# Kernel optimization log

Measured on AMD Instinct MI355X. Metric: run time of the kernel, lower is better.

Reference implementation:

```python
import jax, jax.numpy as jnp
import numpy as np

B, S, D, H, V = 4, 2048, 128, 4, 64
HD = D // H
ITERS = 3
SCALE = 1.0 / float(np.sqrt(HD))
APO = 0.2
TRP = 0.15
FC = 1.61803
EPS = 1e-5


def ln(x, g, b):
    m = x.mean(-1, keepdims=True)
    v = ((x - m) ** 2).mean(-1, keepdims=True)
    return (x - m) / jnp.sqrt(v + EPS) * g + b


def setup_inputs() -> dict:
    key = jax.random.key(0)
    ks = iter(jax.random.split(key, 64))

    def w(shape, s=0.02):
        return jax.random.normal(next(ks), shape, jnp.float32) * s

    return {
        "x": jax.random.normal(next(ks), (B, S, D), jnp.float32),
        "space": jax.random.normal(next(ks), (B, S, D), jnp.float32),
        # attn_norm
        "g_attn": jnp.ones(D), "b_attn": jnp.zeros(D),
        # RecursiveScaledDotProductAttention
        "Wq": w((D, D)), "Wk": w((D, D)), "Wv": w((D, D)),
        "Wo": w((D, D)), "bo": jnp.zeros(D),
        "Wg": w((D, 2 * D)), "bg": jnp.zeros(D),
        "Wobs": w((H, D)), "bobs": jnp.zeros(H),
        # trp_norm + TraumaResolutionPathLayer
        "g_trp": jnp.ones(D), "b_trp": jnp.zeros(D),
        "Wt": w((V, D)), "bt": jnp.zeros(V),
        "Wc": w((V, D)), "bc": jnp.zeros(V),
        "Ws": w((V, D)), "bs": jnp.zeros(V),
        "Wr": w((V, 3 * V)), "br": jnp.zeros(V),
        "fv": jnp.ones(V) * FC,
        "Wop": w((D, V)), "bop": jnp.zeros(D),
        # MorphogenesisFFN
        "g_ffn": jnp.ones(D), "b_ffn": jnp.zeros(D),
        "W1": w((4 * D, D)), "b1": jnp.zeros(4 * D),
        "W2": w((D, 4 * D)), "b2": jnp.zeros(D),
        "Wsg": w((D, D)), "bsg": jnp.zeros(D),
        # ApophasisLayer
        "g_apo": jnp.ones(D), "b_apo": jnp.zeros(D),
        "Wn": w((D, D)), "bn": jnp.zeros(D),
    }


def reference(x, space, g_attn, b_attn, Wq, Wk, Wv, Wo, bo, Wg, bg, Wobs, bobs,
              g_trp, b_trp, Wt, bt, Wc, bc, Ws, bs, Wr, br, fv, Wop, bop,
              g_ffn, b_ffn, W1, b1, W2, b2, Wsg, bsg, g_apo, b_apo, Wn, bn):
    # --- recursive attention (autopoiesis loop, eval mode: dropout = identity) ---
    xn = ln(x, g_attn, b_attn)
    obs = xn.mean(1, keepdims=True)                      # [B,1,D] observer_state default
    infl = (obs @ Wobs.T + bobs).transpose(0, 2, 1)[..., None]  # [B,H,1,1] per-head bias
    cur = xn
    for _ in range(ITERS):
        q = (cur @ Wq.T).reshape(B, S, H, HD).transpose(0, 2, 1, 3)
        k = (cur @ Wk.T).reshape(B, S, H, HD).transpose(0, 2, 1, 3)
        v = (cur @ Wv.T).reshape(B, S, H, HD).transpose(0, 2, 1, 3)
        scores = jnp.einsum('bhqd,bhkd->bhqk', q, k) * SCALE + infl
        aw = jax.nn.softmax(scores, axis=-1)             # [B,H,S,S]
        ao = jnp.einsum('bhqk,bhkd->bhqd', aw, v).transpose(0, 2, 1, 3).reshape(B, S, D)
        out = ao @ Wo.T + bo
        gate = jax.nn.sigmoid(jnp.concatenate([cur, out], -1) @ Wg.T + bg)
        cur = cur * (1 - gate) + out * gate
    x = x + cur
    # --- Trauma Resolution Path ---
    xn2 = ln(x, g_trp, b_trp)
    tv = xn2 @ Wt.T + bt                                 # [B,S,V]
    cv = jnp.broadcast_to(xn2.mean(1, keepdims=True) @ Wc.T + bc, tv.shape)
    sv = space @ Ws.T + bs
    rgate = jax.nn.sigmoid(jnp.concatenate([tv, cv, sv], -1) @ Wr.T + br)
    cn = jnp.maximum(jnp.linalg.norm(cv, axis=-1, keepdims=True), 1e-8)
    sn = jnp.maximum(jnp.linalg.norm(sv, axis=-1, keepdims=True), 1e-8)
    align = (cv * sv).sum(-1, keepdims=True) / (cn * sn)
    resolved = tv + TRP * (-align * (fv - tv) * rgate)
    x = x + resolved @ Wop.T + bop
    # --- Morphogenesis FFN ---
    xn3 = ln(x, g_ffn, b_ffn)
    ff = jax.nn.gelu(xn3 @ W1.T + b1, approximate=False) @ W2.T + b2
    x = x + jax.nn.sigmoid(xn3 @ Wsg.T + bsg) * ff
    # --- Apophasis ---
    x = x - APO * jnp.tanh(ln(x, g_apo, b_apo) @ Wn.T + bn)
    return x, aw
```

## Files before the change

kernel.cpp:

```cpp
#include <hip/hip_runtime.h>
#include <cstdint>
#include <cstddef>


typedef unsigned short u16;
typedef __attribute__((ext_vector_type(8))) short short8;
typedef __attribute__((ext_vector_type(4))) float f32x4;
typedef __attribute__((ext_vector_type(2))) unsigned uint32x2;

#define B_ 4
#define S_ 2048
#define D_ 128
#define H_ 4
#define M_ 8192
#define SCALE2_ 0.25503472510324417f
#define APO_ 0.2f
#define TRP_ 0.15f
#define EPS_ 1e-5f

__device__ __forceinline__ float fexp2(float x){ return __builtin_amdgcn_exp2f(x); }

__device__ __forceinline__ u16 f2bf(float f){
  unsigned u = __float_as_uint(f);
  unsigned r = ((u >> 16) & 1u) + 0x7fffu;
  return (u16)((u + r) >> 16);
}
__device__ __forceinline__ float bf2f(u16 u){ return __uint_as_float(((unsigned)u) << 16); }
__device__ __forceinline__ float sigm(float x){ return 1.0f/(1.0f + __expf(-x)); }

__device__ __forceinline__ unsigned cvtpk_bf16(float lo, float hi){
  unsigned r;
  asm("v_cvt_pk_bf16_f32 %0, %1, %2" : "=v"(r) : "v"(lo), "v"(hi));
  return r;
}

#define LDS_BARRIER() __asm__ volatile("s_waitcnt lgkmcnt(0)\n\ts_barrier" ::: "memory")

struct WSrc { const float* s[13]; };
__global__ __launch_bounds__(256) void prep_k(WSrc w, u16* __restrict__ dst,
    const float* __restrict__ x_in, const float* __restrict__ g,
    const float* __restrict__ b, u16* __restrict__ cg0){
  if (blockIdx.x < 1168){
    int idx = blockIdx.x*256 + threadIdx.x;
    if (idx >= 299008) return;
    const int sz[13] = {16384,16384,16384,16384,32768,8192,8192,12288,8192,65536,65536,16384,16384};
    int off = idx;
    #pragma unroll
    for (int seg = 0; seg < 13; ++seg){
      if (off < sz[seg]) { dst[idx] = f2bf(w.s[seg][off]); return; }
      off -= sz[seg];
    }
  } else {
    int wv = threadIdx.x >> 6, lane = threadIdx.x & 63;
    int row = (blockIdx.x - 1168)*4 + wv;
    size_t rb = (size_t)row * D_;
    float v0 = x_in[rb + lane], v1 = x_in[rb + lane + 64];
    float s = v0 + v1;
    #pragma unroll
    for (int m = 1; m < 64; m <<= 1) s += __shfl_xor(s, m, 64);
    float mean = s * (1.0f/128.0f);
    float d0 = v0 - mean, d1 = v1 - mean;
    float vv = d0*d0 + d1*d1;
    #pragma unroll
    for (int m = 1; m < 64; m <<= 1) vv += __shfl_xor(vv, m, 64);
    float rstd = rsqrtf(vv * (1.0f/128.0f) + EPS_);
    cg0[rb + lane]      = f2bf(d0*rstd*g[lane]    + b[lane]);
    cg0[rb + lane + 64] = f2bf(d1*rstd*g[lane+64] + b[lane+64]);
  }
}

__global__ __launch_bounds__(256) void ln_kernel(const float* __restrict__ in0,
    const u16* __restrict__ in1bf, const float* __restrict__ g, const float* __restrict__ b,
    float* __restrict__ sumout, u16* __restrict__ ybf){
  int wv = threadIdx.x >> 6, lane = threadIdx.x & 63;
  int row = blockIdx.x*4 + wv;
  size_t rb = (size_t)row * D_;
  float v0 = in0[rb + lane], v1 = in0[rb + lane + 64];
  if (in1bf){ v0 += bf2f(in1bf[rb + lane]); v1 += bf2f(in1bf[rb + lane + 64]); }
  if (sumout){ sumout[rb + lane] = v0; sumout[rb + lane + 64] = v1; }
  float s = v0 + v1;
  #pragma unroll
  for (int m = 1; m < 64; m <<= 1) s += __shfl_xor(s, m, 64);
  float mean = s * (1.0f/128.0f);
  float d0 = v0 - mean, d1 = v1 - mean;
  float vv = d0*d0 + d1*d1;
  #pragma unroll
  for (int m = 1; m < 64; m <<= 1) vv += __shfl_xor(vv, m, 64);
  float rstd = rsqrtf(vv * (1.0f/128.0f) + EPS_);
  ybf[rb + lane]      = f2bf(d0*rstd*g[lane]    + b[lane]);
  ybf[rb + lane + 64] = f2bf(d1*rstd*g[lane+64] + b[lane+64]);
}

__global__ __launch_bounds__(256) void colmean_k(const u16* __restrict__ lnb,
    const float* __restrict__ Wc, const float* __restrict__ bc,
    float* __restrict__ cv, float* __restrict__ cn){
  __shared__ float red[2][128];
  __shared__ float cmS[128];
  int b = blockIdx.x;
  int d = threadIdx.x & 127, sc = threadIdx.x >> 7;
  const u16* pp = lnb + (size_t)b*S_*D_ + (size_t)sc*1024*D_ + d;
  float s = 0.f;
  #pragma unroll 8
  for (int i = 0; i < 1024; ++i) s += bf2f(pp[(size_t)i*D_]);
  red[sc][d] = s;
  __syncthreads();
  if (sc == 0) cmS[d] = (red[0][d] + red[1][d]) * (1.0f/2048.0f);
  __syncthreads();
  int tid = threadIdx.x;
  if (tid < 64){
    int n = tid;
    const float* wrow = Wc + n*D_;
    float sacc = bc[n];
    #pragma unroll 4
    for (int dd = 0; dd < D_; ++dd) sacc += cmS[dd]*wrow[dd];
    cv[b*64 + n] = sacc;
    float sq = sacc*sacc;
    #pragma unroll
    for (int m = 1; m < 64; m <<= 1) sq += __shfl_xor(sq, m, 64);
    if (n == 0) cn[b] = fmaxf(sqrtf(sq), 1e-8f);
  }
}

__global__ __launch_bounds__(256) void gemm_qkv(const u16* __restrict__ A,
    const u16* __restrict__ W, u16* __restrict__ qh, u16* __restrict__ kh, u16* __restrict__ vt){
  __shared__ u16 Asm[64*136];
  __shared__ u16 Bsm[64*136];
  const int m0 = blockIdx.x*64, n0 = blockIdx.y*64;
  int tid = threadIdx.x;
  int wv = tid >> 6, lane = tid & 63, quad = lane >> 4, l15 = lane & 15;
  int wm = wv >> 1, wn = wv & 1;
  {
    int sr = tid >> 2, cb = (tid & 3)*32;
    const u16* ag = A + (size_t)(m0 + sr)*128 + cb;
    const u16* bg = W + (size_t)(n0 + sr)*128 + cb;
    short8 a0 = *(const short8*)(ag + 0);
    short8 a1 = *(const short8*)(ag + 8);
    short8 a2 = *(const short8*)(ag + 16);
    short8 a3 = *(const short8*)(ag + 24);
    short8 b0 = *(const short8*)(bg + 0);
    short8 b1 = *(const short8*)(bg + 8);
    short8 b2 = *(const short8*)(bg + 16);
    short8 b3 = *(const short8*)(bg + 24);
    *(short8*)(Asm + sr*136 + cb + 0)  = a0;
    *(short8*)(Asm + sr*136 + cb + 8)  = a1;
    *(short8*)(Asm + sr*136 + cb + 16) = a2;
    *(short8*)(Asm + sr*136 + cb + 24) = a3;
    *(short8*)(Bsm + sr*136 + cb + 0)  = b0;
    *(short8*)(Bsm + sr*136 + cb + 8)  = b1;
    *(short8*)(Bsm + sr*136 + cb + 16) = b2;
    *(short8*)(Bsm + sr*136 + cb + 24) = b3;
  }
  LDS_BARRIER();
  f32x4 acc[2][2];
  #pragma unroll
  for (int i = 0; i < 2; ++i)
    #pragma unroll
    for (int j = 0; j < 2; ++j) acc[i][j] = (f32x4){0.f,0.f,0.f,0.f};
  #pragma unroll
  for (int k0 = 0; k0 < 128; k0 += 32){
    short8 af0 = *(const short8*)(Asm + (wm*32      + l15)*136 + k0 + quad*8);
    short8 af1 = *(const short8*)(Asm + (wm*32 + 16 + l15)*136 + k0 + quad*8);
    short8 bf0 = *(const short8*)(Bsm + (wn*32      + l15)*136 + k0 + quad*8);
    short8 bf1 = *(const short8*)(Bsm + (wn*32 + 16 + l15)*136 + k0 + quad*8);
    acc[0][0] = __builtin_amdgcn_mfma_f32_16x16x32_bf16(af0, bf0, acc[0][0], 0,0,0);
    acc[0][1] = __builtin_amdgcn_mfma_f32_16x16x32_bf16(af0, bf1, acc[0][1], 0,0,0);
    acc[1][0] = __builtin_amdgcn_mfma_f32_16x16x32_bf16(af1, bf0, acc[1][0], 0,0,0);
    acc[1][1] = __builtin_amdgcn_mfma_f32_16x16x32_bf16(af1, bf1, acc[1][1], 0,0,0);
  }
  #pragma unroll
  for (int ms = 0; ms < 2; ++ms)
    #pragma unroll
    for (int ns = 0; ns < 2; ++ns){
      int mb = m0 + wm*32 + ms*16 + quad*4;
      int nn = n0 + wn*32 + ns*16 + l15;
      int which = nn >> 7, col = nn & 127, h = col >> 5, hd = col & 31;
      f32x4 c = acc[ms][ns];
      #pragma unroll
      for (int r = 0; r < 4; ++r){
        int m = mb + r, b = m >> 11, s = m & 2047;
        if (which == 0)      qh[((size_t)(b*H_+h)*S_ + s)*32 + hd] = f2bf(c[r]);
        else if (which == 1) kh[((size_t)(b*H_+h)*S_ + s)*32 + hd] = f2bf(c[r]);
        else                 vt[((size_t)(b*H_+h)*32 + hd)*S_ + s] = f2bf(c[r]);
      }
    }
}

template<bool WRITE_AW>
__global__ __launch_bounds__(256) void attn_k(const u16* __restrict__ qh, const u16* __restrict__ kh,
    const u16* __restrict__ vT, u16* __restrict__ ao_bf, float* __restrict__ aw){
  __shared__ u16 Ks[2][128*40];
  __shared__ u16 Vs[2][32*136];
  __shared__ u16 Ps[4*16*136];
  int L = blockIdx.y*32 + blockIdx.x;
  int xcd = L & 7, j = L >> 3;
  int bh = 2*xcd + (j >> 5);
  int q0 = (j & 31)*64;
  int b = bh >> 2, h = bh & 3;
  int tid = threadIdx.x, wv = tid >> 6, lane = tid & 63, quad = lane >> 4, l15 = lane & 15;
  int qrow = q0 + wv*16 + l15;
  const size_t bhS = (size_t)bh * S_;
  short8 qf = *(const short8*)(qh + (bhS + qrow)*32 + quad*8);
  int krow = tid >> 1, kseg = (tid & 1)*16;
  const u16* kg = kh + (bhS + krow)*32 + kseg;
  int vrow = tid >> 3, vseg = (tid & 7)*16;
  const u16* vg = vT + ((size_t)bh*32 + vrow)*S_ + vseg;
  f32x4 zero = {0.f,0.f,0.f,0.f};
  f32x4 ao0 = zero, ao1 = zero;
  float lsum = 0.f, rinv = 1.0f;
  u16* PsW = Ps + wv*16*136;

  if constexpr (WRITE_AW){
    {
      short8 a0 = *(const short8*)(kg + 0);
      short8 a1 = *(const short8*)(kg + 8);
      *(short8*)(Ks[0] + krow*40 + kseg    ) = a0;
      *(short8*)(Ks[0] + krow*40 + kseg + 8) = a1;
    }
    #pragma unroll 2
    for (int t = 0; t < 16; ++t){
      LDS_BARRIER();
      short8 n0, n1;
      if (t < 15){
        n0 = *(const short8*)(kg + (size_t)(t+1)*4096 + 0);
        n1 = *(const short8*)(kg + (size_t)(t+1)*4096 + 8);
      }
      const u16* Kb = Ks[t & 1];
      #pragma unroll
      for (int jt = 0; jt < 8; ++jt){
        short8 kf = *(const short8*)(Kb + (jt*16 + l15)*40 + quad*8);
        f32x4 s = __builtin_amdgcn_mfma_f32_16x16x32_bf16(kf, qf, zero, 0,0,0);
        #pragma unroll
        for (int r = 0; r < 4; ++r) lsum += fexp2(s[r]*SCALE2_);
      }
      if (t < 15){
        u16* Kn = Ks[(t+1) & 1];
        *(short8*)(Kn + krow*40 + kseg    ) = n0;
        *(short8*)(Kn + krow*40 + kseg + 8) = n1;
      }
    }
    lsum += __shfl_xor(lsum, 16, 64);
    lsum += __shfl_xor(lsum, 32, 64);
    rinv = 1.0f / lsum;
  }

  {
    short8 a0 = *(const short8*)(kg + 0);
    short8 a1 = *(const short8*)(kg + 8);
    short8 b0 = *(const short8*)(vg + 0);
    short8 b1 = *(const short8*)(vg + 8);
    *(short8*)(Ks[0] + krow*40 + kseg    ) = a0;
    *(short8*)(Ks[0] + krow*40 + kseg + 8) = a1;
    *(short8*)(Vs[0] + vrow*136 + vseg    ) = b0;
    *(short8*)(Vs[0] + vrow*136 + vseg + 8) = b1;
  }
  #pragma unroll 2
  for (int t = 0; t < 16; ++t){
    LDS_BARRIER();
    short8 kn0, kn1, vn0, vn1;
    if (t < 15){
      kn0 = *(const short8*)(kg + (size_t)(t+1)*4096 + 0);
      kn1 = *(const short8*)(kg + (size_t)(t+1)*4096 + 8);
      vn0 = *(const short8*)(vg + (size_t)(t+1)*128 + 0);
      vn1 = *(const short8*)(vg + (size_t)(t+1)*128 + 8);
    }
    const u16* Kb = Ks[t & 1];
    const u16* Vb = Vs[t & 1];
    int k0 = t*128;
    #pragma unroll
    for (int jt = 0; jt < 8; ++jt){
      short8 kf = *(const short8*)(Kb + (jt*16 + l15)*40 + quad*8);
      f32x4 s = __builtin_amdgcn_mfma_f32_16x16x32_bf16(kf, qf, zero, 0,0,0);
      float pv[4];
      #pragma unroll
      for (int r = 0; r < 4; ++r){
        float e = fexp2(s[r]*SCALE2_);
        if constexpr (WRITE_AW) e *= rinv; else lsum += e;
        pv[r] = e;
      }
      if constexpr (WRITE_AW){
        f32x4 st = {pv[0], pv[1], pv[2], pv[3]};
        *(f32x4*)(aw + (bhS + qrow)*S_ + k0 + jt*16 + quad*4) = st;
      }
      uint32x2 pk;
      pk[0] = cvtpk_bf16(pv[0], pv[1]);
      pk[1] = cvtpk_bf16(pv[2], pv[3]);
      *(uint32x2*)(PsW + l15*136 + jt*16 + quad*4) = pk;
    }
    __asm__ volatile("s_waitcnt lgkmcnt(0)" ::: "memory");
    #pragma unroll
    for (int jg = 0; jg < 4; ++jg){
      short8 pf  = *(const short8*)(PsW + l15*136 + jg*32 + quad*8);
      short8 vf0 = *(const short8*)(Vb + (l15     )*136 + jg*32 + quad*8);
      short8 vf1 = *(const short8*)(Vb + (16 + l15)*136 + jg*32 + quad*8);
      ao0 = __builtin_amdgcn_mfma_f32_16x16x32_bf16(vf0, pf, ao0, 0,0,0);
      ao1 = __builtin_amdgcn_mfma_f32_16x16x32_bf16(vf1, pf, ao1, 0,0,0);
    }
    if (t < 15){
      u16* Kn = Ks[(t+1) & 1];
      u16* Vn = Vs[(t+1) & 1];
      *(short8*)(Kn + krow*40 + kseg    ) = kn0;
      *(short8*)(Kn + krow*40 + kseg + 8) = kn1;
      *(short8*)(Vn + vrow*136 + vseg    ) = vn0;
      *(short8*)(Vn + vrow*136 + vseg + 8) = vn1;
    }
  }

  if constexpr (!WRITE_AW){
    lsum += __shfl_xor(lsum, 16, 64);
    lsum += __shfl_xor(lsum, 32, 64);
    rinv = 1.0f / lsum;
  } else rinv = 1.0f;

  size_t rowbase = ((size_t)(b*S_ + qrow))*D_ + h*32;
  #pragma unroll
  for (int dt = 0; dt < 2; ++dt){
    f32x4 a = dt ? ao1 : ao0;
    uint32x2 pk;
    pk[0] = cvtpk_bf16(a[0]*rinv, a[1]*rinv);
    pk[1] = cvtpk_bf16(a[2]*rinv, a[3]*rinv);
    *(uint32x2*)(ao_bf + rowbase + dt*16 + quad*4) = pk;
  }
}

template<bool DO_QKV>
__global__ __launch_bounds__(256) void wqkv_k(const u16* __restrict__ cin,
    const u16* __restrict__ ao_bf, const u16* __restrict__ wo, const u16* __restrict__ wg,
    const u16* __restrict__ w3, const float* __restrict__ bo, const float* __restrict__ bg,
    u16* __restrict__ cout, u16* __restrict__ qh, u16* __restrict__ kh, u16* __restrict__ vt){
  __shared__ u16 aoS[16*136];
  __shared__ u16 cuS[16*136];
  __shared__ u16 outS[16*136];
  __shared__ u16 coS[16*136];
  const int m0 = blockIdx.x*16;
  int tid = threadIdx.x, wv = tid >> 6, lane = tid & 63, quad = lane >> 4, l15 = lane & 15;
  {
    int row = tid >> 4, seg = (tid & 15)*8;
    *(short8*)(aoS + row*136 + seg) = *(const short8*)(ao_bf + (size_t)(m0+row)*128 + seg);
    *(short8*)(cuS + row*136 + seg) = *(const short8*)(cin   + (size_t)(m0+row)*128 + seg);
  }
  __syncthreads();
  f32x4 oacc[2] = {(f32x4){0,0,0,0},(f32x4){0,0,0,0}};
  #pragma unroll
  for (int kc = 0; kc < 4; ++kc){
    short8 af = *(const short8*)(aoS + l15*136 + kc*32 + quad*8);
    #pragma unroll
    for (int nt = 0; nt < 2; ++nt){
      int n = wv*32 + nt*16 + l15;
      short8 bfv = *(const short8*)(wo + (size_t)n*128 + kc*32 + quad*8);
      oacc[nt] = __builtin_amdgcn_mfma_f32_16x16x32_bf16(af, bfv, oacc[nt], 0,0,0);
    }
  }
  #pragma unroll
  for (int nt = 0; nt < 2; ++nt){
    int n = wv*32 + nt*16 + l15;
    float bias = bo[n];
    #pragma unroll
    for (int r = 0; r < 4; ++r){
      int m = quad*4 + r;
      outS[m*136 + n] = f2bf(oacc[nt][r] + bias);
    }
  }
  __syncthreads();
  f32x4 gacc[2] = {(f32x4){0,0,0,0},(f32x4){0,0,0,0}};
  #pragma unroll
  for (int kc = 0; kc < 8; ++kc){
    short8 af = (kc < 4) ? *(const short8*)(cuS  + l15*136 + kc*32 + quad*8)
                         : *(const short8*)(outS + l15*136 + (kc-4)*32 + quad*8);
    #pragma unroll
    for (int nt = 0; nt < 2; ++nt){
      int n = wv*32 + nt*16 + l15;
      short8 bfv = *(const short8*)(wg + (size_t)n*256 + kc*32 + quad*8);
      gacc[nt] = __builtin_amdgcn_mfma_f32_16x16x32_bf16(af, bfv, gacc[nt], 0,0,0);
    }
  }
  #pragma unroll
  for (int nt = 0; nt < 2; ++nt){
    int n = wv*32 + nt*16 + l15;
    float biasg = bg[n], biaso = bo[n];
    #pragma unroll
    for (int r = 0; r < 4; ++r){
      int m = quad*4 + r;
      float g = sigm(gacc[nt][r] + biasg);
      float c = bf2f(cuS[m*136 + n]);
      float o = oacc[nt][r] + biaso;
      u16 val = f2bf(c + g*(o - c));
      cout[(size_t)(m0+m)*128 + n] = val;
      if constexpr (DO_QKV) coS[m*136 + n] = val;
    }
  }
  if constexpr (DO_QKV){
    __syncthreads();
    f32x4 qacc[6];
    #pragma unroll
    for (int i = 0; i < 6; ++i) qacc[i] = (f32x4){0,0,0,0};
    #pragma unroll
    for (int kc = 0; kc < 4; ++kc){
      short8 af = *(const short8*)(coS + l15*136 + kc*32 + quad*8);
      #pragma unroll
      for (int nt = 0; nt < 6; ++nt){
        int n = wv*96 + nt*16 + l15;
        short8 bfv = *(const short8*)(w3 + (size_t)n*128 + kc*32 + quad*8);
        qacc[nt] = __builtin_amdgcn_mfma_f32_16x16x32_bf16(af, bfv, qacc[nt], 0,0,0);
      }
    }
    #pragma unroll
    for (int nt = 0; nt < 6; ++nt){
      int nn = wv*96 + nt*16 + l15;
      int which = nn >> 7, col = nn & 127, h = col >> 5, hd = col & 31;
      #pragma unroll
      for (int r = 0; r < 4; ++r){
        int m = m0 + quad*4 + r, b = m >> 11, s = m & 2047;
        if (which == 0)      qh[((size_t)(b*H_+h)*S_ + s)*32 + hd] = f2bf(qacc[nt][r]);
        else if (which == 1) kh[((size_t)(b*H_+h)*S_ + s)*32 + hd] = f2bf(qacc[nt][r]);
        else                 vt[((size_t)(b*H_+h)*32 + hd)*S_ + s] = f2bf(qacc[nt][r]);
      }
    }
  }
}

__global__ __launch_bounds__(256) void uber_k(const u16* __restrict__ lnb,
    const float* __restrict__ space, const float* __restrict__ xbuf,
    const float* __restrict__ cv, const float* __restrict__ cn,
    const u16* __restrict__ wt, const float* __restrict__ bt,
    const u16* __restrict__ wsx, const float* __restrict__ bs,
    const u16* __restrict__ wr, const float* __restrict__ br, const float* __restrict__ fv,
    const u16* __restrict__ wop, const float* __restrict__ bop,
    const float* __restrict__ g_ffn, const float* __restrict__ b_ffn,
    const u16* __restrict__ w1, const float* __restrict__ b1,
    const u16* __restrict__ w2, const float* __restrict__ b2,
    const u16* __restrict__ wsg, const float* __restrict__ bsg,
    const float* __restrict__ g_apo, const float* __restrict__ b_apo,
    const u16* __restrict__ wn, const float* __restrict__ bn,
    float* __restrict__ out_x){
  __shared__ u16 xnS[16*136];
  __shared__ u16 spS[16*136];
  __shared__ u16 CcS[16*200];
  __shared__ float svF[16*64];
  __shared__ u16 RsS[16*72];
  __shared__ float xrF[16*128];
  __shared__ u16 midS[16*536];
  __shared__ float alignS[16];
  const int m0 = blockIdx.x*16;
  const int bidx = m0 >> 11;
  int tid = threadIdx.x, wv = tid >> 6, lane = tid & 63, quad = lane >> 4, l15 = lane & 15;

  {
    int row = tid >> 4, seg = (tid & 15)*8;
    *(short8*)(xnS + row*136 + seg) = *(const short8*)(lnb + (size_t)(m0+row)*128 + seg);
    const float* sp = space + (size_t)(m0+row)*128 + seg;
    short8 pk;
    #pragma unroll
    for (int i = 0; i < 8; ++i) pk[i] = (short)f2bf(sp[i]);
    *(short8*)(spS + row*136 + seg) = pk;
    f32x4 xa = *(const f32x4*)(xbuf + (size_t)(m0+row)*128 + seg);
    f32x4 xb = *(const f32x4*)(xbuf + (size_t)(m0+row)*128 + seg + 4);
    *(f32x4*)(xrF + row*128 + seg) = xa;
    *(f32x4*)(xrF + row*128 + seg + 4) = xb;
  }
  __syncthreads();

  f32x4 tvacc = {0,0,0,0};
  {
    int n = wv*16 + l15;
    #pragma unroll
    for (int kc = 0; kc < 4; ++kc){
      short8 af  = *(const short8*)(xnS + l15*136 + kc*32 + quad*8);
      short8 bfv = *(const short8*)(wt + (size_t)n*128 + kc*32 + quad*8);
      tvacc = __builtin_amdgcn_mfma_f32_16x16x32_bf16(af, bfv, tvacc, 0,0,0);
    }
    float bias = bt[n];
    #pragma unroll
    for (int r = 0; r < 4; ++r){
      tvacc[r] += bias;
      CcS[(quad*4 + r)*200 + n] = f2bf(tvacc[r]);
    }
  }
  {
    int n = wv*16 + l15;
    f32x4 sva = {0,0,0,0};
    #pragma unroll
    for (int kc = 0; kc < 4; ++kc){
      short8 af  = *(const short8*)(spS + l15*136 + kc*32 + quad*8);
      short8 bfv = *(const short8*)(wsx + (size_t)n*128 + kc*32 + quad*8);
      sva = __builtin_amdgcn_mfma_f32_16x16x32_bf16(af, bfv, sva, 0,0,0);
    }
    float bias = bs[n];
    #pragma unroll
    for (int r = 0; r < 4; ++r){
      float v = sva[r] + bias;
      int m = quad*4 + r;
      CcS[m*200 + 128 + n] = f2bf(v);
      svF[m*64 + n] = v;
    }
    int row = tid >> 4, c4 = (tid & 15)*4;
    #pragma unroll
    for (int i = 0; i < 4; ++i)
      CcS[row*200 + 64 + c4 + i] = f2bf(cv[bidx*64 + c4 + i]);
  }
  __syncthreads();

  {
    float cnb = cn[bidx];
    for (int rr = wv*4; rr < wv*4 + 4; ++rr){
      float s = svF[rr*64 + lane];
      float c = cv[bidx*64 + lane];
      float dot = c*s, ss = s*s;
      #pragma unroll
      for (int m = 1; m < 64; m <<= 1){ dot += __shfl_xor(dot, m, 64); ss += __shfl_xor(ss, m, 64); }
      if (lane == 0){
        float sn = fmaxf(sqrtf(ss), 1e-8f);
        alignS[rr] = dot / (cnb * sn);
      }
    }
  }
  __syncthreads();

  {
    int n = wv*16 + l15;
    f32x4 ra = {0,0,0,0};
    #pragma unroll
    for (int kc = 0; kc < 6; ++kc){
      short8 af  = *(const short8*)(CcS + l15*200 + kc*32 + quad*8);
      short8 bfv = *(const short8*)(wr + (size_t)n*192 + kc*32 + quad*8);
      ra = __builtin_amdgcn_mfma_f32_16x16x32_bf16(af, bfv, ra, 0,0,0);
    }
    float bias = br[n], fvn = fv[n];
    #pragma unroll
    for (int r = 0; r < 4; ++r){
      int m = quad*4 + r;
      float rg = sigm(ra[r] + bias);
      float t = tvacc[r];
      float res = t + TRP_*(-alignS[m]*(fvn - t)*rg);
      RsS[m*72 + n] = f2bf(res);
    }
  }
  __syncthreads();

  {
    f32x4 wa[2] = {(f32x4){0,0,0,0},(f32x4){0,0,0,0}};
    #pragma unroll
    for (int kc = 0; kc < 2; ++kc){
      short8 af = *(const short8*)(RsS + l15*72 + kc*32 + quad*8);
      #pragma unroll
      for (int nt = 0; nt < 2; ++nt){
        int n = wv*32 + nt*16 + l15;
        short8 bfv = *(const short8*)(wop + (size_t)n*64 + kc*32 + quad*8);
        wa[nt] = __builtin_amdgcn_mfma_f32_16x16x32_bf16(af, bfv, wa[nt], 0,0,0);
      }
    }
    #pragma unroll
    for (int nt = 0; nt < 2; ++nt){
      int n = wv*32 + nt*16 + l15;
      float bias = bop[n];
      #pragma unroll
      for (int r = 0; r < 4; ++r){
        int m = quad*4 + r;
        xrF[m*128 + n] += wa[nt][r] + bias;
      }
    }
  }
  __syncthreads();

  for (int rr = wv*4; rr < wv*4 + 4; ++rr){
    float v0 = xrF[rr*128 + lane], v1 = xrF[rr*128 + lane + 64];
    float s = v0 + v1;
    #pragma unroll
    for (int m = 1; m < 64; m <<= 1) s += __shfl_xor(s, m, 64);
    float mean = s * (1.0f/128.0f);
    float d0 = v0 - mean, d1 = v1 - mean;
    float vvv = d0*d0 + d1*d1;
    #pragma unroll
    for (int m = 1; m < 64; m <<= 1) vvv += __shfl_xor(vvv, m, 64);
    float rstd = rsqrtf(vvv * (1.0f/128.0f) + EPS_);
    xnS[rr*136 + lane]      = f2bf(d0*rstd*g_ffn[lane]    + b_ffn[lane]);
    xnS[rr*136 + lane + 64] = f2bf(d1*rstd*g_ffn[lane+64] + b_ffn[lane+64]);
  }
  __syncthreads();

  {
    f32x4 acc[8];
    #pragma unroll
    for (int i = 0; i < 8; ++i) acc[i] = (f32x4){0,0,0,0};
    #pragma unroll
    for (int kc = 0; kc < 4; ++kc){
      short8 af = *(const short8*)(xnS + l15*136 + kc*32 + quad*8);
      #pragma unroll
      for (int nt = 0; nt < 8; ++nt){
        int n = wv*128 + nt*16 + l15;
        short8 bfv = *(const short8*)(w1 + (size_t)n*128 + kc*32 + quad*8);
        acc[nt] = __builtin_amdgcn_mfma_f32_16x16x32_bf16(af, bfv, acc[nt], 0,0,0);
      }
    }
    #pragma unroll
    for (int nt = 0; nt < 8; ++nt){
      int n = wv*128 + nt*16 + l15;
      float bias = b1[n];
      #pragma unroll
      for (int r = 0; r < 4; ++r){
        int m = quad*4 + r;
        float lin = acc[nt][r] + bias;
        float ge = 0.5f*lin*(1.0f + erff(lin*0.70710678118654752f));
        midS[m*536 + n] = f2bf(ge);
      }
    }
  }
  __syncthreads();

  {
    f32x4 ffa[2] = {(f32x4){0,0,0,0},(f32x4){0,0,0,0}};
    #pragma unroll
    for (int kc = 0; kc < 16; ++kc){
      short8 af = *(const short8*)(midS + l15*536 + kc*32 + quad*8);
      #pragma unroll
      for (int nt = 0; nt < 2; ++nt){
        int n = wv*32 + nt*16 + l15;
        short8 bfv = *(const short8*)(w2 + (size_t)n*512 + kc*32 + quad*8);
        ffa[nt] = __builtin_amdgcn_mfma_f32_16x16x32_bf16(af, bfv, ffa[nt], 0,0,0);
      }
    }
    f32x4 sga[2] = {(f32x4){0,0,0,0},(f32x4){0,0,0,0}};
    #pragma unroll
    for (int kc = 0; kc < 4; ++kc){
      short8 af = *(const short8*)(xnS + l15*136 + kc*32 + quad*8);
      #pragma unroll
      for (int nt = 0; nt < 2; ++nt){
        int n = wv*32 + nt*16 + l15;
        short8 bfv = *(const short8*)(wsg + (size_t)n*128 + kc*32 + quad*8);
        sga[nt] = __builtin_amdgcn_mfma_f32_16x16x32_bf16(af, bfv, sga[nt], 0,0,0);
      }
    }
    #pragma unroll
    for (int nt = 0; nt < 2; ++nt){
      int n = wv*32 + nt*16 + l15;
      float b2n = b2[n], bsgn = bsg[n];
      #pragma unroll
      for (int r = 0; r < 4; ++r){
        int m = quad*4 + r;
        float ff = ffa[nt][r] + b2n;
        float sg = sigm(sga[nt][r] + bsgn);
        xrF[m*128 + n] += sg*ff;
      }
    }
  }
  __syncthreads();

  for (int rr = wv*4; rr < wv*4 + 4; ++rr){
    float v0 = xrF[rr*128 + lane], v1 = xrF[rr*128 + lane + 64];
    float s = v0 + v1;
    #pragma unroll
    for (int m = 1; m < 64; m <<= 1) s += __shfl_xor(s, m, 64);
    float mean = s * (1.0f/128.0f);
    float d0 = v0 - mean, d1 = v1 - mean;
    float vvv = d0*d0 + d1*d1;
    #pragma unroll
    for (int m = 1; m < 64; m <<= 1) vvv += __shfl_xor(vvv, m, 64);
    float rstd = rsqrtf(vvv * (1.0f/128.0f) + EPS_);
    xnS[rr*136 + lane]      = f2bf(d0*rstd*g_apo[lane]    + b_apo[lane]);
    xnS[rr*136 + lane + 64] = f2bf(d1*rstd*g_apo[lane+64] + b_apo[lane+64]);
  }
  __syncthreads();

  {
    f32x4 na[2] = {(f32x4){0,0,0,0},(f32x4){0,0,0,0}};
    #pragma unroll
    for (int kc = 0; kc < 4; ++kc){
      short8 af = *(const short8*)(xnS + l15*136 + kc*32 + quad*8);
      #pragma unroll
      for (int nt = 0; nt < 2; ++nt){
        int n = wv*32 + nt*16 + l15;
        short8 bfv = *(const short8*)(wn + (size_t)n*128 + kc*32 + quad*8);
        na[nt] = __builtin_amdgcn_mfma_f32_16x16x32_bf16(af, bfv, na[nt], 0,0,0);
      }
    }
    #pragma unroll
    for (int nt = 0; nt < 2; ++nt){
      int n = wv*32 + nt*16 + l15;
      float bias = bn[n];
      #pragma unroll
      for (int r = 0; r < 4; ++r){
        int m = quad*4 + r;
        out_x[(size_t)(m0+m)*128 + n] = xrF[m*128 + n] - APO_*tanhf(na[nt][r] + bias);
      }
    }
  }
}

extern "C" void kernel_launch(void* const* d_in, const int* in_sizes, int n_in,
                              void* d_out, int out_size, void* d_ws, size_t ws_size,
                              hipStream_t stream){
  (void)in_sizes; (void)n_in; (void)out_size; (void)ws_size;
  const float* x_in   = (const float*)d_in[0];
  const float* space  = (const float*)d_in[1];
  const float* g_attn = (const float*)d_in[2];
  const float* b_attn = (const float*)d_in[3];
  const float* Wq     = (const float*)d_in[4];
  const float* Wk     = (const float*)d_in[5];
  const float* Wv     = (const float*)d_in[6];
  const float* Wo     = (const float*)d_in[7];
  const float* bo     = (const float*)d_in[8];
  const float* Wg     = (const float*)d_in[9];
  const float* bg     = (const float*)d_in[10];
  const float* g_trp  = (const float*)d_in[13];
  const float* b_trp  = (const float*)d_in[14];
  const float* Wt     = (const float*)d_in[15];
  const float* bt     = (const float*)d_in[16];
  const float* Wc     = (const float*)d_in[17];
  const float* bc     = (const float*)d_in[18];
  const float* Ws_    = (const float*)d_in[19];
  const float* bs     = (const float*)d_in[20];
  const float* Wr     = (const float*)d_in[21];
  const float* br     = (const float*)d_in[22];
  const float* fv     = (const float*)d_in[23];
  const float* Wop    = (const float*)d_in[24];
  const float* bop    = (const float*)d_in[25];
  const float* g_ffn  = (const float*)d_in[26];
  const float* b_ffn  = (const float*)d_in[27];
  const float* W1_    = (const float*)d_in[28];
  const float* b1     = (const float*)d_in[29];
  const float* W2_    = (const float*)d_in[30];
  const float* b2     = (const float*)d_in[31];
  const float* Wsg_   = (const float*)d_in[32];
  const float* bsg    = (const float*)d_in[33];
  const float* g_apo  = (const float*)d_in[34];
  const float* b_apo  = (const float*)d_in[35];
  const float* Wn_    = (const float*)d_in[36];
  const float* bn     = (const float*)d_in[37];

  char* base = (char*)d_ws;
  size_t off = 0;
  auto alloc = [&](size_t bytes)->char* {
    char* r = base + off; off += (bytes + 255) & ~(size_t)255; return r; };
  u16*  wbf   = (u16*) alloc((size_t)299008*2);
  u16*  cg0   = (u16*) alloc((size_t)M_*D_*2);
  u16*  cg1   = (u16*) alloc((size_t)M_*D_*2);
  u16*  qh    = (u16*) alloc((size_t)16*S_*32*2);
  u16*  kh    = (u16*) alloc((size_t)16*S_*32*2);
  u16*  vt    = (u16*) alloc((size_t)16*32*S_*2);
  u16*  ao_bf = (u16*) alloc((size_t)M_*D_*2);
  u16*  lnb   = (u16*) alloc((size_t)M_*D_*2);
  float* xbuf = (float*)alloc((size_t)M_*D_*4);
  float* cvb  = (float*)alloc(4*64*4);
  float* cnb  = (float*)alloc(4*4);

  u16* wqkv = wbf;
  u16* wo   = wbf + 49152;
  u16* wg   = wbf + 65536;
  u16* wt   = wbf + 98304;
  u16* wsx  = wbf + 106496;
  u16* wr   = wbf + 114688;
  u16* wop  = wbf + 126976;
  u16* w1   = wbf + 135168;
  u16* w2   = wbf + 200704;
  u16* wsgp = wbf + 266240;
  u16* wn   = wbf + 282624;

  float* out_x = (float*)d_out;
  float* aw    = out_x + (size_t)M_*D_;

  WSrc wsrc;
  wsrc.s[0]=Wq; wsrc.s[1]=Wk; wsrc.s[2]=Wv; wsrc.s[3]=Wo; wsrc.s[4]=Wg;
  wsrc.s[5]=Wt; wsrc.s[6]=Ws_; wsrc.s[7]=Wr; wsrc.s[8]=Wop; wsrc.s[9]=W1_;
  wsrc.s[10]=W2_; wsrc.s[11]=Wsg_; wsrc.s[12]=Wn_;

  prep_k<<<1168 + M_/4, 256, 0, stream>>>(wsrc, wbf, x_in, g_attn, b_attn, cg0);
  gemm_qkv<<<dim3(M_/64, 6), 256, 0, stream>>>(cg0, wqkv, qh, kh, vt);

  attn_k<false><<<dim3(S_/64, 16), 256, 0, stream>>>(qh, kh, vt, ao_bf, nullptr);
  wqkv_k<true ><<<M_/16, 256, 0, stream>>>(cg0, ao_bf, wo, wg, wqkv, bo, bg, cg1, qh, kh, vt);
  attn_k<false><<<dim3(S_/64, 16), 256, 0, stream>>>(qh, kh, vt, ao_bf, nullptr);
  wqkv_k<true ><<<M_/16, 256, 0, stream>>>(cg1, ao_bf, wo, wg, wqkv, bo, bg, cg0, qh, kh, vt);
  attn_k<true ><<<dim3(S_/64, 16), 256, 0, stream>>>(qh, kh, vt, ao_bf, aw);
  wqkv_k<false><<<M_/16, 256, 0, stream>>>(cg0, ao_bf, wo, wg, wqkv, bo, bg, cg1, qh, kh, vt);

  ln_kernel<<<M_/4, 256, 0, stream>>>(x_in, cg1, g_trp, b_trp, xbuf, lnb);
  colmean_k<<<4, 256, 0, stream>>>(lnb, Wc, bc, cvb, cnb);

  uber_k<<<M_/16, 256, 0, stream>>>(lnb, space, xbuf, cvb, cnb,
      wt, bt, wsx, bs, wr, br, fv, wop, bop,
      g_ffn, b_ffn, w1, b1, w2, b2, wsgp, bsg,
      g_apo, b_apo, wn, bn, out_x);
}
```

Before: 247.4 us.

## Fuse residual+LayerNorm into final gate kernel, widen colmean, fold softmax normalization into exp

Removes the standalone ln_kernel by computing the residual add and trp LayerNorm inside the last wqkv_k launch from the gated output held in shared memory, which avoids a kernel launch and a round trip of cur through global memory. colmean_k now uses 512 threads with vectorized 8-wide bf16 loads and a 32-way shared reduction instead of a 2-way split of strided scalar loads. The attention-weight pass folds the 1/sum normalization into the exp2 argument as a log2 offset, replacing a multiply with an fma. The last-iteration kernel no longer writes cg1 to global memory.

```diff
diff --git a/kernel.cpp b/kernel.cpp
--- a/kernel.cpp
+++ b/kernel.cpp
@@ -69,44 +69,34 @@
   }
 }
 
-__global__ __launch_bounds__(256) void ln_kernel(const float* __restrict__ in0,
-    const u16* __restrict__ in1bf, const float* __restrict__ g, const float* __restrict__ b,
-    float* __restrict__ sumout, u16* __restrict__ ybf){
-  int wv = threadIdx.x >> 6, lane = threadIdx.x & 63;
-  int row = blockIdx.x*4 + wv;
-  size_t rb = (size_t)row * D_;
-  float v0 = in0[rb + lane], v1 = in0[rb + lane + 64];
-  if (in1bf){ v0 += bf2f(in1bf[rb + lane]); v1 += bf2f(in1bf[rb + lane + 64]); }
-  if (sumout){ sumout[rb + lane] = v0; sumout[rb + lane + 64] = v1; }
-  float s = v0 + v1;
-  #pragma unroll
-  for (int m = 1; m < 64; m <<= 1) s += __shfl_xor(s, m, 64);
-  float mean = s * (1.0f/128.0f);
-  float d0 = v0 - mean, d1 = v1 - mean;
-  float vv = d0*d0 + d1*d1;
-  #pragma unroll
-  for (int m = 1; m < 64; m <<= 1) vv += __shfl_xor(vv, m, 64);
-  float rstd = rsqrtf(vv * (1.0f/128.0f) + EPS_);
-  ybf[rb + lane]      = f2bf(d0*rstd*g[lane]    + b[lane]);
-  ybf[rb + lane + 64] = f2bf(d1*rstd*g[lane+64] + b[lane+64]);
-}
-
-__global__ __launch_bounds__(256) void colmean_k(const u16* __restrict__ lnb,
+__global__ __launch_bounds__(512) void colmean_k(const u16* __restrict__ lnb,
     const float* __restrict__ Wc, const float* __restrict__ bc,
     float* __restrict__ cv, float* __restrict__ cn){
-  __shared__ float red[2][128];
+  __shared__ float red2[32][128];
   __shared__ float cmS[128];
   int b = blockIdx.x;
-  int d = threadIdx.x & 127, sc = threadIdx.x >> 7;
-  const u16* pp = lnb + (size_t)b*S_*D_ + (size_t)sc*1024*D_ + d;
-  float s = 0.f;
-  #pragma unroll 8
-  for (int i = 0; i < 1024; ++i) s += bf2f(pp[(size_t)i*D_]);
-  red[sc][d] = s;
-  __syncthreads();
-  if (sc == 0) cmS[d] = (red[0][d] + red[1][d]) * (1.0f/2048.0f);
-  __syncthreads();
   int tid = threadIdx.x;
+  int rg = tid >> 4, c8 = (tid & 15)*8;
+  const u16* pp = lnb + (size_t)b*S_*D_ + (size_t)rg*D_ + c8;
+  float acc[8];
+  #pragma unroll
+  for (int j = 0; j < 8; ++j) acc[j] = 0.f;
+  #pragma unroll 4
+  for (int i = 0; i < 64; ++i){
+    short8 v = *(const short8*)(pp + (size_t)i*32*D_);
+    #pragma unroll
+    for (int j = 0; j < 8; ++j) acc[j] += bf2f((u16)v[j]);
+  }
+  #pragma unroll
+  for (int j = 0; j < 8; ++j) red2[rg][c8 + j] = acc[j];
+  __syncthreads();
+  if (tid < 128){
+    float s = 0.f;
+    #pragma unroll
+    for (int r = 0; r < 32; ++r) s += red2[r][tid];
+    cmS[tid] = s * (1.0f/2048.0f);
+  }
+  __syncthreads();
   if (tid < 64){
     int n = tid;
     const float* wrow = Wc + n*D_;
@@ -206,7 +196,7 @@
   const u16* vg = vT + ((size_t)bh*32 + vrow)*S_ + vseg;
   f32x4 zero = {0.f,0.f,0.f,0.f};
   f32x4 ao0 = zero, ao1 = zero;
-  float lsum = 0.f, rinv = 1.0f;
+  float lsum = 0.f, rinv = 1.0f, nls = 0.f;
   u16* PsW = Ps + wv*16*136;
 
   if constexpr (WRITE_AW){
@@ -240,7 +230,7 @@
     }
     lsum += __shfl_xor(lsum, 16, 64);
     lsum += __shfl_xor(lsum, 32, 64);
-    rinv = 1.0f / lsum;
+    nls = -__log2f(lsum);
   }
 
   {
@@ -273,8 +263,9 @@
       float pv[4];
       #pragma unroll
       for (int r = 0; r < 4; ++r){
-        float e = fexp2(s[r]*SCALE2_);
-        if constexpr (WRITE_AW) e *= rinv; else lsum += e;
+        float e;
+        if constexpr (WRITE_AW) e = fexp2(__builtin_fmaf(s[r], SCALE2_, nls));
+        else { e = fexp2(s[r]*SCALE2_); lsum += e; }
         pv[r] = e;
       }
       if constexpr (WRITE_AW){
@@ -309,7 +300,7 @@
     lsum += __shfl_xor(lsum, 16, 64);
     lsum += __shfl_xor(lsum, 32, 64);
     rinv = 1.0f / lsum;
-  } else rinv = 1.0f;
+  }
 
   size_t rowbase = ((size_t)(b*S_ + qrow))*D_ + h*32;
   #pragma unroll
@@ -326,7 +317,9 @@
 __global__ __launch_bounds__(256) void wqkv_k(const u16* __restrict__ cin,
     const u16* __restrict__ ao_bf, const u16* __restrict__ wo, const u16* __restrict__ wg,
     const u16* __restrict__ w3, const float* __restrict__ bo, const float* __restrict__ bg,
-    u16* __restrict__ cout, u16* __restrict__ qh, u16* __restrict__ kh, u16* __restrict__ vt){
+    u16* __restrict__ cout, u16* __restrict__ qh, u16* __restrict__ kh, u16* __restrict__ vt,
+    const float* __restrict__ x_in, const float* __restrict__ g_trp,
+    const float* __restrict__ b_trp, float* __restrict__ xbuf, u16* __restrict__ lnb){
   __shared__ u16 aoS[16*136];
   __shared__ u16 cuS[16*136];
   __shared__ u16 outS[16*136];
@@ -384,12 +377,12 @@
       float c = bf2f(cuS[m*136 + n]);
       float o = oacc[nt][r] + biaso;
       u16 val = f2bf(c + g*(o - c));
-      cout[(size_t)(m0+m)*128 + n] = val;
-      if constexpr (DO_QKV) coS[m*136 + n] = val;
-    }
-  }
+      coS[m*136 + n] = val;
+      if constexpr (DO_QKV) cout[(size_t)(m0+m)*128 + n] = val;
+    }
+  }
+  __syncthreads();
   if constexpr (DO_QKV){
-    __syncthreads();
     f32x4 qacc[6];
     #pragma unroll
     for (int i = 0; i < 6; ++i) qacc[i] = (f32x4){0,0,0,0};
@@ -414,6 +407,24 @@
         else if (which == 1) kh[((size_t)(b*H_+h)*S_ + s)*32 + hd] = f2bf(qacc[nt][r]);
         else                 vt[((size_t)(b*H_+h)*32 + hd)*S_ + s] = f2bf(qacc[nt][r]);
       }
+    }
+  } else {
+    for (int rr = wv*4; rr < wv*4 + 4; ++rr){
+      size_t rb = (size_t)(m0+rr)*128;
+      float v0 = x_in[rb + lane]      + bf2f(coS[rr*136 + lane]);
+      float v1 = x_in[rb + lane + 64] + bf2f(coS[rr*136 + lane + 64]);
+      xbuf[rb + lane] = v0; xbuf[rb + lane + 64] = v1;
+      float s = v0 + v1;
+      #pragma unroll
+      for (int m = 1; m < 64; m <<= 1) s += __shfl_xor(s, m, 64);
+      float mean = s * (1.0f/128.0f);
+      float d0 = v0 - mean, d1 = v1 - mean;
+      float vv = d0*d0 + d1*d1;
+      #pragma unroll
+      for (int m = 1; m < 64; m <<= 1) vv += __shfl_xor(vv, m, 64);
+      float rstd = rsqrtf(vv * (1.0f/128.0f) + EPS_);
+      lnb[rb + lane]      = f2bf(d0*rstd*g_trp[lane]    + b_trp[lane]);
+      lnb[rb + lane + 64] = f2bf(d1*rstd*g_trp[lane+64] + b_trp[lane+64]);
     }
   }
 }
@@ -766,14 +777,16 @@
   gemm_qkv<<<dim3(M_/64, 6), 256, 0, stream>>>(cg0, wqkv, qh, kh, vt);
 
   attn_k<false><<<dim3(S_/64, 16), 256, 0, stream>>>(qh, kh, vt, ao_bf, nullptr);
-  wqkv_k<true ><<<M_/16, 256, 0, stream>>>(cg0, ao_bf, wo, wg, wqkv, bo, bg, cg1, qh, kh, vt);
+  wqkv_k<true ><<<M_/16, 256, 0, stream>>>(cg0, ao_bf, wo, wg, wqkv, bo, bg, cg1, qh, kh, vt,
+                                           x_in, g_trp, b_trp, xbuf, lnb);
   attn_k<false><<<dim3(S_/64, 16), 256, 0, stream>>>(qh, kh, vt, ao_bf, nullptr);
-  wqkv_k<true ><<<M_/16, 256, 0, stream>>>(cg1, ao_bf, wo, wg, wqkv, bo, bg, cg0, qh, kh, vt);
+  wqkv_k<true ><<<M_/16, 256, 0, stream>>>(cg1, ao_bf, wo, wg, wqkv, bo, bg, cg0, qh, kh, vt,
+                                           x_in, g_trp, b_trp, xbuf, lnb);
   attn_k<true ><<<dim3(S_/64, 16), 256, 0, stream>>>(qh, kh, vt, ao_bf, aw);
-  wqkv_k<false><<<M_/16, 256, 0, stream>>>(cg0, ao_bf, wo, wg, wqkv, bo, bg, cg1, qh, kh, vt);
-
-  ln_kernel<<<M_/4, 256, 0, stream>>>(x_in, cg1, g_trp, b_trp, xbuf, lnb);
-  colmean_k<<<4, 256, 0, stream>>>(lnb, Wc, bc, cvb, cnb);
+  wqkv_k<false><<<M_/16, 256, 0, stream>>>(cg0, ao_bf, wo, wg, wqkv, bo, bg, cg1, qh, kh, vt,
+                                           x_in, g_trp, b_trp, xbuf, lnb);
+
+  colmean_k<<<4, 512, 0, stream>>>(lnb, Wc, bc, cvb, cnb);
 
   uber_k<<<M_/16, 256, 0, stream>>>(lnb, space, xbuf, cvb, cnb,
       wt, bt, wsx, bs, wr, br, fv, wop, bop,
```

After: 214.1 us. 1.16x faster.
